# Performance work log

Hardware: AMD Instinct MI355X
Metric: run time of the kernel (lower is better)

## Reference

```python
import jax, jax.numpy as jnp
import numpy as np
import math

B, T, C = 2, 1024, 1024
H = 16
HS = C // H          # head size 64
ROT = HS // 2        # rotary dims 32
TT = 1024            # ctx_len
FFN = 4 * C
EPS = 1e-6


def _layernorm(x, g, b):
    m = jnp.mean(x, -1, keepdims=True)
    v = jnp.mean((x - m) ** 2, -1, keepdims=True)
    return (x - m) * jax.lax.rsqrt(v + EPS) * g + b


def _time_shift_half(x):
    # ZeroPad2d((0,0,1,-1)) applied to first half of channels: shift by one step in time
    c = x.shape[-1]
    a = jnp.pad(x[:, :, : c // 2], ((0, 0), (1, 0), (0, 0)))[:, :-1, :]
    return jnp.concatenate([a, x[:, :, c // 2 :]], axis=-1)


def _rotate_half(x):
    x1, x2 = jnp.split(x, 2, axis=-1)
    return jnp.concatenate([-x2, x1], axis=-1)


def _rotary_cos_sin(t_len, rot, base):
    inv_freq = 1.0 / (base ** (jnp.arange(0, rot, 2, dtype=jnp.float32) / rot))
    freqs = jnp.arange(t_len, dtype=jnp.float32)[:, None] * inv_freq[None, :]
    emb = jnp.concatenate([freqs, freqs], axis=-1)  # (T, rot)
    return jnp.cos(emb), jnp.sin(emb)


def _build_w(time_w, time_alpha, time_beta, t_len):
    # faithful translation of the pad/tile/reshape circulant trick
    w = jnp.pad(time_w, ((0, 0), (0, TT)))            # (H, 2TT)
    w = jnp.tile(w, (1, TT))                          # (H, 2TT*TT)
    w = w[:, :-TT].reshape(-1, TT, 2 * TT - 1)        # (H, TT, 2TT-1)
    w = w[:, :, TT - 1 :]                             # (H, TT, TT)
    return w[:, :t_len, :t_len] * time_alpha[:, :, :t_len] * time_beta[:, :t_len, :]


def setup_inputs() -> dict:
    key = jax.random.key(0)
    ks = jax.random.split(key, 24)
    s = 0.02
    d = {
        "x": jax.random.normal(ks[0], (B, T, C), jnp.float32),
        "ln1_g": jnp.ones((C,), jnp.float32),
        "ln1_b": jnp.zeros((C,), jnp.float32),
        "Wq": jax.random.normal(ks[1], (C, C), jnp.float32) * s,
        "bq": jnp.zeros((C,), jnp.float32),
        "Wk": jax.random.normal(ks[2], (C, C), jnp.float32) * s,
        "bk": jnp.zeros((C,), jnp.float32),
        "Wv": jax.random.normal(ks[3], (C, C), jnp.float32) * s,
        "bv": jnp.zeros((C,), jnp.float32),
        "Wo": jax.random.normal(ks[4], (C, C), jnp.float32) * s,
        "bo": jnp.zeros((C,), jnp.float32),
        "time_w": 1.0 + 0.01 * jax.random.normal(ks[5], (H, TT), jnp.float32),
        "time_alpha": 1.0 + 0.01 * jax.random.normal(ks[6], (H, 1, TT), jnp.float32),
        "time_beta": 1.0 + 0.01 * jax.random.normal(ks[7], (H, TT, 1), jnp.float32),
        "time_gamma": 1.0 + 0.01 * jax.random.normal(ks[8], (TT, 1), jnp.float32),
        "Wmix": jnp.eye(H, dtype=jnp.float32) + 0.01 * jax.random.normal(ks[9], (H, H), jnp.float32),
        "ln2_g": jnp.ones((C,), jnp.float32),
        "ln2_b": jnp.zeros((C,), jnp.float32),
        "Wgk": jax.random.normal(ks[10], (C, FFN), jnp.float32) * s,
        "bgk": jnp.zeros((FFN,), jnp.float32),
        "Wgv": jax.random.normal(ks[11], (C, FFN), jnp.float32) * s,
        "bgv": jnp.zeros((FFN,), jnp.float32),
        "Wgw": jax.random.normal(ks[12], (FFN, C), jnp.float32) * s,
        "bgw": jnp.zeros((C,), jnp.float32),
    }
    return d


def _block(x, ln1_g, ln1_b, Wq, bq, Wk, bk, Wv, bv, Wo, bo,
           time_w, time_alpha, time_beta, time_gamma, Wmix,
           ln2_g, ln2_b, Wgk, bgk, Wgv, bgv, Wgw, bgw):
    b, t, c = x.shape
    # ---- MHA_pro attention sublayer (pre-LN residual) ----
    xs = _time_shift_half(_layernorm(x, ln1_g, ln1_b))
    q = (xs @ Wq + bq).reshape(b, t, H, HS).transpose(0, 2, 1, 3)  # bhtd
    k = (xs @ Wk + bk).reshape(b, t, H, HS).transpose(0, 2, 1, 3)
    v = (xs @ Wv + bv).reshape(b, t, H, HS).transpose(0, 2, 1, 3)
    qr, qp = q[..., :ROT], q[..., ROT:]
    kr, kp = k[..., :ROT], k[..., ROT:]
    cos, sin = _rotary_cos_sin(t, ROT, float(TT))  # base = ctx_len
    qr = qr * cos + _rotate_half(qr) * sin
    kr = kr * cos + _rotate_half(kr) * sin
    q = jnp.concatenate([qr, qp], axis=-1)
    k = jnp.concatenate([kr, kp], axis=-1)
    att = jnp.einsum("bhtd,bhud->bhtu", q, k) * (1.0 / math.sqrt(HS))
    causal = jnp.tril(jnp.ones((t, t), bool))
    att = jnp.where(causal, att, -jnp.inf)
    att = jax.nn.softmax(att, axis=-1)
    w = _build_w(time_w, time_alpha, time_beta, t)  # (H, T, T)
    att = att * w[None]
    att = jnp.einsum("ij,bjtu->bitu", Wmix, att)  # 1x1 conv head mix
    y = jnp.einsum("bhtu,bhud->bhtd", att, v)
    y = y.transpose(0, 2, 1, 3).reshape(b, t, c)
    y = (y @ Wo + bo) * time_gamma[:t, :]
    x = x + y
    # ---- GeGLU MLP sublayer (pre-LN residual) ----
    xm = _layernorm(x, ln2_g, ln2_b)
    kk = xm @ Wgk + bgk
    vv = xm @ Wgv + bgv
    y2 = (jax.nn.gelu(kk, approximate=False) * vv) @ Wgw + bgw
    return x + y2


def reference(x, ln1_g, ln1_b, Wq, bq, Wk, bk, Wv, bv, Wo, bo,
              time_w, time_alpha, time_beta, time_gamma, Wmix,
              ln2_g, ln2_b, Wgk, bgk, Wgv, bgv, Wgw, bgw):
    return _block(x, ln1_g, ln1_b, Wq, bq, Wk, bk, Wv, bv, Wo, bo,
                  time_w, time_alpha, time_beta, time_gamma, Wmix,
                  ln2_g, ln2_b, Wgk, bgk, Wgv, bgv, Wgw, bgw)
```

## Files before the change

kernel.cpp:

```cpp
#include <hip/hip_runtime.h>
#include <math.h>

typedef unsigned short u16;
typedef short s16x8 __attribute__((ext_vector_type(8)));
typedef float f32x4 __attribute__((ext_vector_type(4)));

#define TB 2
#define TSEQ 1024
#define CC 1024
#define NH 16
#define HSZ 64
#define FFN 4096
#define MROWS (TB*TSEQ)

#define GLOAD16(g, l) __builtin_amdgcn_global_load_lds( \
    (const __attribute__((address_space(1))) unsigned*)(g), \
    (__attribute__((address_space(3))) unsigned*)(l), 16, 0, 0)

__device__ __forceinline__ float bf2f(u16 u){
  union { unsigned u; float f; } c; c.u = ((unsigned)u) << 16; return c.f;
}
__device__ __forceinline__ u16 f2bf(float f){
  union { float f; unsigned u; } c; c.f = f;
  unsigned u = c.u;
  u += 0x7fffu + ((u >> 16) & 1);
  return (u16)(u >> 16);
}
__device__ __forceinline__ float ldin(const void* p, size_t i, int bf){
  return bf ? bf2f(((const u16*)p)[i]) : ((const float*)p)[i];
}

__global__ void k_flag(const unsigned* __restrict__ g, int* __restrict__ flag){
  if (threadIdx.x == 0) *flag = (g[0] == 0x3F800000u) ? 0 : 1;
}

__global__ void k_transpose_cvt(const void* __restrict__ in, u16* __restrict__ out,
                                int R, int Cc, const int* __restrict__ flagp){
  int bf = *flagp;
  __shared__ u16 tile[32][33];
  int bx = blockIdx.x * 32, by = blockIdx.y * 32;
  int tx = threadIdx.x & 31, ty = threadIdx.x >> 5;
  #pragma unroll
  for (int i = 0; i < 32; i += 8)
    tile[ty + i][tx] = f2bf(ldin(in, (size_t)(by + ty + i) * Cc + bx + tx, bf));
  __syncthreads();
  #pragma unroll
  for (int i = 0; i < 32; i += 8)
    out[(size_t)(bx + ty + i) * R + by + tx] = tile[tx][ty + i];
}

__global__ void k_cvt(const void* __restrict__ in, u16* __restrict__ out, int n,
                      const int* __restrict__ flagp){
  int bf = *flagp;
  int i = blockIdx.x * 256 + threadIdx.x;
  if (i < n) out[i] = f2bf(ldin(in, i, bf));
}

__global__ void k_tw8(const void* __restrict__ tw, u16* __restrict__ tw8,
                      const int* __restrict__ flagp){
  int bf = *flagp;
  int idx = blockIdx.x*256 + threadIdx.x;
  int s = idx >> 14;
  int h = (idx >> 10) & 15;
  int k = idx & 1023;
  float v = (k + s < 1024) ? ldin(tw, h*1024 + k + s, bf) : 0.f;
  tw8[idx] = f2bf(v);
}

__global__ void k_ln1_shift(const void* __restrict__ x, const void* __restrict__ g,
                            const void* __restrict__ bta, u16* __restrict__ xs,
                            const int* __restrict__ flagp){
  int bf = *flagp;
  int row = blockIdx.x;
  int t = row & (TSEQ - 1);
  int tid = threadIdx.x;
  float v[4]; float s = 0.f, ss = 0.f;
  #pragma unroll
  for (int i = 0; i < 4; i++){
    v[i] = ldin(x, (size_t)row * CC + tid*4 + i, bf);
    s += v[i]; ss += v[i]*v[i];
  }
  __shared__ float rs[256], rss[256];
  rs[tid] = s; rss[tid] = ss; __syncthreads();
  for (int o = 128; o > 0; o >>= 1){ if (tid < o){ rs[tid] += rs[tid+o]; rss[tid] += rss[tid+o]; } __syncthreads(); }
  float mean = rs[0] * (1.0f/CC);
  float var  = rss[0] * (1.0f/CC) - mean*mean;
  float inv  = rsqrtf(var + 1e-6f);
  #pragma unroll
  for (int i = 0; i < 4; i++){
    int c = tid*4 + i;
    float o = (v[i]-mean)*inv*ldin(g, c, bf) + ldin(bta, c, bf);
    u16 ob = f2bf(o);
    if (c >= CC/2)            xs[(size_t)row*CC + c] = ob;
    else if (t < TSEQ-1)      xs[(size_t)(row+1)*CC + c] = ob;
  }
  if (t == 0 && tid < 128){
    #pragma unroll
    for (int i = 0; i < 4; i++) xs[(size_t)row*CC + tid*4 + i] = 0;
  }
}

__global__ void k_ln2(const float* __restrict__ x1, const void* __restrict__ g,
                      const void* __restrict__ bta, u16* __restrict__ xm,
                      const int* __restrict__ flagp){
  int bf = *flagp;
  int row = blockIdx.x;
  int tid = threadIdx.x;
  const float* xr = x1 + (size_t)row * CC;
  float v[4]; float s = 0.f, ss = 0.f;
  #pragma unroll
  for (int i = 0; i < 4; i++){ v[i] = xr[tid*4 + i]; s += v[i]; ss += v[i]*v[i]; }
  __shared__ float rs[256], rss[256];
  rs[tid] = s; rss[tid] = ss; __syncthreads();
  for (int o = 128; o > 0; o >>= 1){ if (tid < o){ rs[tid] += rs[tid+o]; rss[tid] += rss[tid+o]; } __syncthreads(); }
  float mean = rs[0] * (1.0f/CC);
  float var  = rss[0] * (1.0f/CC) - mean*mean;
  float inv  = rsqrtf(var + 1e-6f);
  #pragma unroll
  for (int i = 0; i < 4; i++){
    int c = tid*4 + i;
    xm[(size_t)row*CC + c] = f2bf((v[i]-mean)*inv*ldin(g, c, bf) + ldin(bta, c, bf));
  }
}

__global__ void k_rotary(u16* __restrict__ qkv){
  int idx = blockIdx.x*256 + threadIdx.x;
  int i = idx & 15;
  int h = (idx >> 4) & (NH-1);
  int row = idx >> 8;
  int t = row & (TSEQ-1);
  float invf = exp2f(-0.625f * (float)i);
  float ang = (float)t * invf;
  float cs = cosf(ang), sn = sinf(ang);
  size_t base = (size_t)row * (3*CC);
  u16* qp = qkv + base + h*HSZ;
  float a = bf2f(qp[i]), b2 = bf2f(qp[i+16]);
  qp[i]    = f2bf(a*cs - b2*sn);
  qp[i+16] = f2bf(b2*cs + a*sn);
  u16* kp = qkv + base + CC + h*HSZ;
  a = bf2f(kp[i]); b2 = bf2f(kp[i+16]);
  kp[i]    = f2bf(a*cs - b2*sn);
  kp[i+16] = f2bf(b2*cs + a*sn);
}

__global__ __launch_bounds__(256) void k_qk(
    const u16* __restrict__ qkv, u16* __restrict__ att)
{
  int m0 = blockIdx.y * 128;
  int n0 = blockIdx.x * 128;
  if (n0 > m0) return;
  int bh = blockIdx.z; int b = bh >> 4, h = bh & 15;
  __shared__ u16 As[128*32];
  __shared__ u16 Bs[128*32];
  int tid = threadIdx.x;
  int w = tid >> 6;
  int lane = tid & 63;
  int wm = (w >> 1) * 64, wn = (w & 1) * 64;
  f32x4 acc[4][4];
  #pragma unroll
  for (int i = 0; i < 4; i++)
    #pragma unroll
    for (int j = 0; j < 4; j++) acc[i][j] = (f32x4){0.f,0.f,0.f,0.f};

  int rr = lane >> 2;
  int cc = lane & 3;
  const u16* gA0 = qkv + (size_t)(b*TSEQ + m0 + w*32 + rr)*(3*CC) + h*HSZ + cc*8;
  const u16* gA1 = gA0 + (size_t)16*(3*CC);
  const u16* gB0 = qkv + (size_t)(b*TSEQ + n0 + w*32 + rr)*(3*CC) + CC + h*HSZ + cc*8;
  const u16* gB1 = gB0 + (size_t)16*(3*CC);
  u16* lA0 = As + (w*32)*32;
  u16* lA1 = As + (w*32+16)*32;
  u16* lB0 = Bs + (w*32)*32;
  u16* lB1 = Bs + (w*32+16)*32;
  int quad = lane >> 4;
  int l15 = lane & 15;

  #pragma unroll
  for (int k0 = 0; k0 < HSZ; k0 += 32){
    __syncthreads();
    GLOAD16(gA0 + k0, lA0);
    GLOAD16(gA1 + k0, lA1);
    GLOAD16(gB0 + k0, lB0);
    GLOAD16(gB1 + k0, lB1);
    __syncthreads();
    s16x8 af[4], bfr[4];
    #pragma unroll
    for (int i = 0; i < 4; i++){
      af[i]  = *(s16x8*)&As[(wm + i*16 + l15)*32 + quad*8];
      bfr[i] = *(s16x8*)&Bs[(wn + i*16 + l15)*32 + quad*8];
    }
    #pragma unroll
    for (int mi = 0; mi < 4; mi++)
      #pragma unroll
      for (int ni = 0; ni < 4; ni++)
        acc[mi][ni] = __builtin_amdgcn_mfma_f32_16x16x32_bf16(af[mi], bfr[ni], acc[mi][ni], 0, 0, 0);
  }

  #pragma unroll
  for (int mi = 0; mi < 4; mi++){
    int rowb = m0 + wm + mi*16 + quad*4;
    #pragma unroll
    for (int ni = 0; ni < 4; ni++){
      int col = n0 + wn + ni*16 + l15;
      #pragma unroll
      for (int r = 0; r < 4; r++){
        int t = rowb + r;
        att[((size_t)bh*TSEQ + t)*TSEQ + col] = f2bf(acc[mi][ni][r] * 0.125f);
      }
    }
  }
}

__global__ __launch_bounds__(256) void k_softmix(
    u16* __restrict__ att, const u16* __restrict__ tw8, const u16* __restrict__ al16,
    const u16* __restrict__ be16, const void* __restrict__ wmix,
    const int* __restrict__ flagp)
{
  int bf = *flagp;
  int bt = blockIdx.x;
  int t = bt & (TSEQ-1);
  int b = bt >> 10;
  int tid = threadIdx.x;
  int wv = tid >> 6;
  int lane = tid & 63;
  int tile_end = ((t >> 7) + 1) << 7;
  int nchunk = (t >> 9) + 1;
  int sh = (TSEQ-1 - t) & 7;
  int base = (TSEQ-1 - t) - sh;
  __shared__ __align__(16) u16 P[NH][TSEQ];
  __shared__ float wm[NH*NH];
  if (tid < NH*NH) wm[tid] = ldin(wmix, tid, bf);

  #pragma unroll
  for (int hi = 0; hi < 4; hi++){
    int h = wv*4 + hi;
    const u16* srow = att + ((size_t)(b*NH + h)*TSEQ + t)*TSEQ;
    const u16* twp  = tw8 + ((size_t)sh*NH + h)*TSEQ + base;
    const u16* alp  = al16 + h*TSEQ;
    float v[16];
    float lmax = -1e30f;
    for (int r = 0; r < nchunk; r++){
      int ub = lane*8 + r*512;
      uint4 pk = *(const uint4*)(srow + ub);
      const u16* pe = (const u16*)&pk;
      #pragma unroll
      for (int e = 0; e < 8; e++){
        float s = bf2f(pe[e]);
        if (ub + e > t) s = -1e30f;
        v[r*8+e] = s;
        lmax = fmaxf(lmax, s);
      }
    }
    #pragma unroll
    for (int o = 32; o > 0; o >>= 1) lmax = fmaxf(lmax, __shfl_xor(lmax, o));
    float lsum = 0.f;
    for (int r = 0; r < nchunk; r++){
      #pragma unroll
      for (int e = 0; e < 8; e++){
        float p = __expf(v[r*8+e] - lmax);
        v[r*8+e] = p; lsum += p;
      }
    }
    #pragma unroll
    for (int o = 32; o > 0; o >>= 1) lsum += __shfl_xor(lsum, o);
    float btv = bf2f(be16[h*TSEQ + t]);
    float inv = btv / lsum;
    for (int r = 0; r < nchunk; r++){
      int ub = lane*8 + r*512;
      uint4 wk = *(const uint4*)(twp + ub);
      uint4 ak = *(const uint4*)(alp + ub);
      const u16* we = (const u16*)&wk;
      const u16* ae = (const u16*)&ak;
      u16 tmp[8];
      #pragma unroll
      for (int e = 0; e < 8; e++){
        float p = v[r*8+e] * inv * bf2f(we[e]) * bf2f(ae[e]);
        tmp[e] = f2bf(p);
      }
      *(uint4*)&P[h][ub] = *(uint4*)tmp;
    }
  }
  __syncthreads();

  int u0 = tid * 4;
  if (u0 < tile_end){
    #pragma unroll
    for (int half = 0; half < 2; half++){
      float acc[8][4];
      #pragma unroll
      for (int i = 0; i < 8; i++)
        #pragma unroll
        for (int k = 0; k < 4; k++) acc[i][k] = 0.f;
      #pragma unroll
      for (int j = 0; j < 16; j++){
        uint2 pk = *(const uint2*)&P[j][u0];
        float p0 = bf2f((u16)(pk.x & 0xffff)), p1 = bf2f((u16)(pk.x >> 16));
        float p2 = bf2f((u16)(pk.y & 0xffff)), p3 = bf2f((u16)(pk.y >> 16));
        #pragma unroll
        for (int i2 = 0; i2 < 8; i2++){
          float w = wm[(half*8 + i2)*NH + j];
          acc[i2][0] += w*p0; acc[i2][1] += w*p1; acc[i2][2] += w*p2; acc[i2][3] += w*p3;
        }
      }
      #pragma unroll
      for (int i2 = 0; i2 < 8; i2++){
        int i = half*8 + i2;
        u16 tmp[4] = {f2bf(acc[i2][0]), f2bf(acc[i2][1]), f2bf(acc[i2][2]), f2bf(acc[i2][3])};
        *(uint2*)(att + ((size_t)(b*NH + i)*TSEQ + t)*TSEQ + u0) = *(uint2*)tmp;
      }
    }
  }
}

__global__ void k_vt(const u16* __restrict__ qkv, u16* __restrict__ vt){
  __shared__ u16 tile[32][33];
  int bh = blockIdx.z; int b = bh >> 4, h = bh & 15;
  int u0 = blockIdx.x * 32, d0 = blockIdx.y * 32;
  int tx = threadIdx.x & 31, ty = threadIdx.x >> 5;
  #pragma unroll
  for (int i = 0; i < 32; i += 8)
    tile[ty + i][tx] = qkv[(size_t)(b*TSEQ + u0 + ty + i)*(3*CC) + 2*CC + h*HSZ + d0 + tx];
  __syncthreads();
  #pragma unroll
  for (int i = 0; i < 32; i += 8)
    vt[((size_t)bh*HSZ + d0 + ty + i)*TSEQ + u0 + tx] = tile[tx][ty + i];
}

__global__ void k_gelumul(const u16* __restrict__ kkvv, u16* __restrict__ hh){
  int idx = blockIdx.x*256 + threadIdx.x;
  int m = idx >> 9;
  int j = (idx & 511) * 8;
  uint4 kk4 = *(const uint4*)(kkvv + (size_t)m*(2*FFN) + j);
  uint4 vv4 = *(const uint4*)(kkvv + (size_t)m*(2*FFN) + FFN + j);
  const u16* ks = (const u16*)&kk4;
  const u16* vs = (const u16*)&vv4;
  u16 out[8];
  #pragma unroll
  for (int e = 0; e < 8; e++){
    float kk = bf2f(ks[e]), vv = bf2f(vs[e]);
    float ge = 0.5f*kk*(1.0f + erff(kk*0.70710678f));
    out[e] = f2bf(ge*vv);
  }
  *(uint4*)(hh + (size_t)m*FFN + j) = *(uint4*)out;
}

__global__ __launch_bounds__(256) void k_gemm(
    const u16* __restrict__ A, const u16* __restrict__ Bt,
    const u16* __restrict__ bias, int M, int N, int K, int mode,
    void* __restrict__ outp, const void* __restrict__ xres,
    const float* __restrict__ resf, const u16* __restrict__ gamma,
    float* __restrict__ partial, const int* __restrict__ flagp)
{
  int bf = *flagp;
  __shared__ u16 As[128*32];
  __shared__ u16 Bs[128*32];
  int tid = threadIdx.x;
  int m0 = blockIdx.y * 128;
  int n0 = blockIdx.x * 128;
  int nz = gridDim.z;
  int kper = K / nz;
  int kbeg = blockIdx.z * kper;
  int kend = kbeg + kper;
  int w = tid >> 6;
  int lane = tid & 63;
  int wm = (w >> 1) * 64, wn = (w & 1) * 64;
  f32x4 acc[4][4];
  #pragma unroll
  for (int i = 0; i < 4; i++)
    #pragma unroll
    for (int j = 0; j < 4; j++) acc[i][j] = (f32x4){0.f,0.f,0.f,0.f};

  int rr = lane >> 2;
  int cc = lane & 3;
  const u16* gA0 = A  + (size_t)(m0 + w*32 + rr)*K + cc*8;
  const u16* gA1 = gA0 + (size_t)16*K;
  const u16* gB0 = Bt + (size_t)(n0 + w*32 + rr)*K + cc*8;
  const u16* gB1 = gB0 + (size_t)16*K;
  u16* lA0 = As + (w*32)*32;
  u16* lA1 = As + (w*32+16)*32;
  u16* lB0 = Bs + (w*32)*32;
  u16* lB1 = Bs + (w*32+16)*32;
  int quad = lane >> 4;
  int l15 = lane & 15;

  for (int k0 = kbeg; k0 < kend; k0 += 32){
    __syncthreads();
    GLOAD16(gA0 + k0, lA0);
    GLOAD16(gA1 + k0, lA1);
    GLOAD16(gB0 + k0, lB0);
    GLOAD16(gB1 + k0, lB1);
    __syncthreads();
    s16x8 af[4], bfr[4];
    #pragma unroll
    for (int i = 0; i < 4; i++){
      af[i]  = *(s16x8*)&As[(wm + i*16 + l15)*32 + quad*8];
      bfr[i] = *(s16x8*)&Bs[(wn + i*16 + l15)*32 + quad*8];
    }
    #pragma unroll
    for (int mi = 0; mi < 4; mi++)
      #pragma unroll
      for (int ni = 0; ni < 4; ni++)
        acc[mi][ni] = __builtin_amdgcn_mfma_f32_16x16x32_bf16(af[mi], bfr[ni], acc[mi][ni], 0, 0, 0);
  }

  if (nz > 1){
    float* pout = partial + (size_t)blockIdx.z * M * N;
    #pragma unroll
    for (int mi = 0; mi < 4; mi++){
      int rowb = m0 + wm + mi*16 + quad*4;
      #pragma unroll
      for (int ni = 0; ni < 4; ni++){
        int col = n0 + wn + ni*16 + l15;
        #pragma unroll
        for (int r = 0; r < 4; r++)
          pout[(size_t)(rowb + r) * N + col] = acc[mi][ni][r];
      }
    }
    return;
  }

  #pragma unroll
  for (int mi = 0; mi < 4; mi++){
    int rowb = m0 + wm + mi*16 + quad*4;
    #pragma unroll
    for (int ni = 0; ni < 4; ni++){
      int col = n0 + wn + ni*16 + l15;
      float bv = bf2f(bias[col]);
      #pragma unroll
      for (int r = 0; r < 4; r++){
        int row = rowb + r;
        float val = acc[mi][ni][r] + bv;
        size_t idx = (size_t)row * N + col;
        if (mode == 0){
          ((u16*)outp)[idx] = f2bf(val);
        } else if (mode == 1){
          int t = row & (TSEQ-1);
          ((float*)outp)[idx] = ldin(xres, idx, bf) + val * bf2f(gamma[t]);
        } else {
          float o = resf[idx] + val;
          if (bf) ((u16*)outp)[idx] = f2bf(o);
          else    ((float*)outp)[idx] = o;
        }
      }
    }
  }
}

__global__ void k_reduceK(const float* __restrict__ partial, int nsplit,
                          int M, int N, const u16* __restrict__ bias, int mode,
                          void* __restrict__ outp, const void* __restrict__ xres,
                          const float* __restrict__ resf, const u16* __restrict__ gamma,
                          const int* __restrict__ flagp){
  int bf = *flagp;
  int idx = blockIdx.x*256 + threadIdx.x;
  int row = idx / (N/4);
  int c0  = (idx % (N/4)) * 4;
  size_t base = (size_t)row * N + c0;
  float v[4] = {0.f, 0.f, 0.f, 0.f};
  for (int s = 0; s < nsplit; s++){
    const float4 p = *(const float4*)(partial + (size_t)s * M * N + base);
    v[0] += p.x; v[1] += p.y; v[2] += p.z; v[3] += p.w;
  }
  #pragma unroll
  for (int e = 0; e < 4; e++) v[e] += bf2f(bias[c0 + e]);
  if (mode == 1){
    int t = row & (TSEQ-1);
    float gm = bf2f(gamma[t]);
    float o[4];
    #pragma unroll
    for (int e = 0; e < 4; e++) o[e] = ldin(xres, base + e, bf) + v[e] * gm;
    *(float4*)((float*)outp + base) = (float4){o[0], o[1], o[2], o[3]};
  } else {
    float o[4];
    #pragma unroll
    for (int e = 0; e < 4; e++) o[e] = resf[base + e] + v[e];
    if (bf){
      u16 tmp[4] = {f2bf(o[0]), f2bf(o[1]), f2bf(o[2]), f2bf(o[3])};
      *(uint2*)((u16*)outp + base) = *(uint2*)tmp;
    } else {
      *(float4*)((float*)outp + base) = (float4){o[0], o[1], o[2], o[3]};
    }
  }
}

__global__ __launch_bounds__(256) void k_pv(
    const u16* __restrict__ att, const u16* __restrict__ vt, u16* __restrict__ y)
{
  __shared__ u16 As[128*32];
  __shared__ u16 Bs[64*32];
  int tid = threadIdx.x;
  int bh = blockIdx.y; int b = bh >> 4, h = bh & 15;
  int m0 = blockIdx.x * 128;
  const u16* A  = att + (size_t)bh * TSEQ * TSEQ;
  const u16* Bt = vt  + (size_t)bh * HSZ * TSEQ;
  int w = tid >> 6;
  int lane = tid & 63;
  int wm = (w >> 1) * 64, wn = (w & 1) * 32;
  f32x4 acc[4][2];
  #pragma unroll
  for (int i = 0; i < 4; i++){ acc[i][0] = (f32x4){0,0,0,0}; acc[i][1] = (f32x4){0,0,0,0}; }

  int rr = lane >> 2;
  int cc = lane & 3;
  const u16* gA0 = A + (size_t)(m0 + w*32 + rr)*TSEQ + cc*8;
  const u16* gA1 = gA0 + (size_t)16*TSEQ;
  const u16* gB0 = Bt + (size_t)(w*16 + rr)*TSEQ + cc*8;
  u16* lA0 = As + (w*32)*32;
  u16* lA1 = As + (w*32+16)*32;
  u16* lB0 = Bs + (w*16)*32;
  int quad = lane >> 4;
  int l15 = lane & 15;
  int kend = m0 + 128;

  for (int k0 = 0; k0 < kend; k0 += 32){
    __syncthreads();
    GLOAD16(gA0 + k0, lA0);
    GLOAD16(gA1 + k0, lA1);
    GLOAD16(gB0 + k0, lB0);
    __syncthreads();
    s16x8 af[4], bfr[2];
    #pragma unroll
    for (int i = 0; i < 4; i++)
      af[i] = *(s16x8*)&As[(wm + i*16 + l15)*32 + quad*8];
    #pragma unroll
    for (int i = 0; i < 2; i++)
      bfr[i] = *(s16x8*)&Bs[(wn + i*16 + l15)*32 + quad*8];
    #pragma unroll
    for (int mi = 0; mi < 4; mi++)
      #pragma unroll
      for (int ni = 0; ni < 2; ni++)
        acc[mi][ni] = __builtin_amdgcn_mfma_f32_16x16x32_bf16(af[mi], bfr[ni], acc[mi][ni], 0, 0, 0);
  }

  #pragma unroll
  for (int mi = 0; mi < 4; mi++){
    int rowb = m0 + wm + mi*16 + quad*4;
    #pragma unroll
    for (int ni = 0; ni < 2; ni++){
      int col = wn + ni*16 + l15;
      #pragma unroll
      for (int r = 0; r < 4; r++){
        int t = rowb + r;
        y[(size_t)(b*TSEQ + t)*CC + h*HSZ + col] = f2bf(acc[mi][ni][r]);
      }
    }
  }
}

extern "C" void kernel_launch(void* const* d_in, const int* in_sizes, int n_in,
                              void* d_out, int out_size, void* d_ws, size_t ws_size,
                              hipStream_t stream){
  const void* x     = d_in[0];
  const void* ln1g  = d_in[1];
  const void* ln1b  = d_in[2];
  const void* Wq    = d_in[3];
  const void* bq    = d_in[4];
  const void* Wk    = d_in[5];
  const void* bk    = d_in[6];
  const void* Wv    = d_in[7];
  const void* bv    = d_in[8];
  const void* Wo    = d_in[9];
  const void* bo    = d_in[10];
  const void* timew = d_in[11];
  const void* alpha = d_in[12];
  const void* beta  = d_in[13];
  const void* gamma = d_in[14];
  const void* Wmix  = d_in[15];
  const void* ln2g  = d_in[16];
  const void* ln2b  = d_in[17];
  const void* Wgk   = d_in[18];
  const void* bgk   = d_in[19];
  const void* Wgv   = d_in[20];
  const void* bgv   = d_in[21];
  const void* Wgw   = d_in[22];
  const void* bgw   = d_in[23];

  char* ws = (char*)d_ws;
  size_t off = 0;
  auto carve = [&](size_t bytes)->char*{
    char* p = ws + off; off = (off + bytes + 255) & ~(size_t)255; return p;
  };
  int*  FLAG   = (int*)carve(256);
  u16*  WT_QKV = (u16*)carve(3072ull*1024*2);
  u16*  WT_O   = (u16*)carve(1024ull*1024*2);
  u16*  WT_G   = (u16*)carve(8192ull*1024*2);
  u16*  WT_W   = (u16*)carve(1024ull*4096*2);
  u16*  B_QKV  = (u16*)carve(3072*2);
  u16*  B_G    = (u16*)carve(8192*2);
  u16*  B_O    = (u16*)carve(1024*2);
  u16*  B_W    = (u16*)carve(1024*2);
  u16*  GMA    = (u16*)carve(1024*2);
  u16*  TW8    = (u16*)carve(8ull*16*1024*2 + 4096);
  u16*  AL16   = (u16*)carve(16*1024*2);
  u16*  BE16   = (u16*)carve(16*1024*2);
  u16*  XS     = (u16*)carve((size_t)MROWS*CC*2);
  u16*  QKV    = (u16*)carve((size_t)MROWS*3*CC*2);
  u16*  ATT    = (u16*)carve((size_t)TB*NH*TSEQ*TSEQ*2);
  u16*  VT     = (u16*)carve((size_t)TB*NH*HSZ*TSEQ*2);
  u16*  Y      = (u16*)carve((size_t)MROWS*CC*2);
  float* X1    = (float*)carve((size_t)MROWS*CC*4);
  u16*  XM     = (u16*)carve((size_t)MROWS*CC*2);
  u16*  KKVV   = (u16*)carve((size_t)MROWS*2*FFN*2);
  u16*  HH     = (u16*)carve((size_t)MROWS*FFN*2);
  float* PART  = (float*)ATT;
  (void)ws_size; (void)in_sizes; (void)n_in; (void)out_size;

  k_flag<<<1,64,0,stream>>>((const unsigned*)ln1g, FLAG);

  k_transpose_cvt<<<dim3(32,32),256,0,stream>>>(Wq, WT_QKV,                1024, 1024, FLAG);
  k_transpose_cvt<<<dim3(32,32),256,0,stream>>>(Wk, WT_QKV + 1024*1024,    1024, 1024, FLAG);
  k_transpose_cvt<<<dim3(32,32),256,0,stream>>>(Wv, WT_QKV + 2*1024*1024,  1024, 1024, FLAG);
  k_transpose_cvt<<<dim3(32,32),256,0,stream>>>(Wo, WT_O,                  1024, 1024, FLAG);
  k_transpose_cvt<<<dim3(128,32),256,0,stream>>>(Wgk, WT_G,                1024, 4096, FLAG);
  k_transpose_cvt<<<dim3(128,32),256,0,stream>>>(Wgv, WT_G + 4096ull*1024, 1024, 4096, FLAG);
  k_transpose_cvt<<<dim3(32,128),256,0,stream>>>(Wgw, WT_W,                4096, 1024, FLAG);
  k_cvt<<<4,256,0,stream>>>(bq, B_QKV,        1024, FLAG);
  k_cvt<<<4,256,0,stream>>>(bk, B_QKV + 1024, 1024, FLAG);
  k_cvt<<<4,256,0,stream>>>(bv, B_QKV + 2048, 1024, FLAG);
  k_cvt<<<16,256,0,stream>>>(bgk, B_G,        4096, FLAG);
  k_cvt<<<16,256,0,stream>>>(bgv, B_G + 4096, 4096, FLAG);
  k_cvt<<<4,256,0,stream>>>(bo,  B_O, 1024, FLAG);
  k_cvt<<<4,256,0,stream>>>(bgw, B_W, 1024, FLAG);
  k_cvt<<<4,256,0,stream>>>(gamma, GMA, 1024, FLAG);
  k_tw8<<<512,256,0,stream>>>(timew, TW8, FLAG);
  k_cvt<<<64,256,0,stream>>>(alpha, AL16, 16384, FLAG);
  k_cvt<<<64,256,0,stream>>>(beta,  BE16, 16384, FLAG);

  k_ln1_shift<<<MROWS,256,0,stream>>>(x, ln1g, ln1b, XS, FLAG);
  k_gemm<<<dim3(24,16),256,0,stream>>>(XS, WT_QKV, B_QKV, MROWS, 3072, 1024, 0,
                                       QKV, nullptr, nullptr, nullptr, nullptr, FLAG);
  k_rotary<<<2048,256,0,stream>>>(QKV);
  k_qk<<<dim3(8,8,TB*NH),256,0,stream>>>(QKV, ATT);
  k_softmix<<<TB*TSEQ,256,0,stream>>>(ATT, TW8, AL16, BE16, Wmix, FLAG);
  k_vt<<<dim3(32,2,32),256,0,stream>>>(QKV, VT);
  k_pv<<<dim3(8,32),256,0,stream>>>(ATT, VT, Y);

  k_gemm<<<dim3(8,16,2),256,0,stream>>>(Y, WT_O, B_O, MROWS, 1024, 1024, 1,
                                        nullptr, nullptr, nullptr, nullptr, PART, FLAG);
  k_reduceK<<<MROWS*1024/(4*256),256,0,stream>>>(PART, 2, MROWS, 1024, B_O, 1,
                                                 X1, x, nullptr, GMA, FLAG);

  k_ln2<<<MROWS,256,0,stream>>>(X1, ln2g, ln2b, XM, FLAG);
  k_gemm<<<dim3(64,16),256,0,stream>>>(XM, WT_G, B_G, MROWS, 8192, 1024, 0,
                                       KKVV, nullptr, nullptr, nullptr, nullptr, FLAG);
  k_gelumul<<<(MROWS*FFN)/(256*8),256,0,stream>>>(KKVV, HH);

  k_gemm<<<dim3(8,16,4),256,0,stream>>>(HH, WT_W, B_W, MROWS, 1024, 4096, 2,
                                        nullptr, nullptr, nullptr, nullptr, PART, FLAG);
  k_reduceK<<<MROWS*1024/(4*256),256,0,stream>>>(PART, 4, MROWS, 1024, B_W, 2,
                                                 d_out, nullptr, X1, nullptr, FLAG);
}
```

Baseline: 477.6 us.

## Fuse GeGLU into gate GEMM epilogue and LN2 into split-K reduction

Interleaves the Wgk and Wgv weight columns in 64-wide blocks so each 128-column GEMM tile holds matching k and v halves. The GELU-times-v product is then computed in the GEMM epilogue through shared memory, which removes the KKVV intermediate buffer and the separate gelumul kernel. The split-K reduction for the output projection also applies the residual, gamma and LayerNorm 2, replacing two kernels with one. The cost is an extra 34KB of LDS in the gate GEMM, which may lower occupancy.

```diff
diff --git a/kernel.cpp b/kernel.cpp
--- a/kernel.cpp
+++ b/kernel.cpp
@@ -35,7 +35,8 @@
 }
 
 __global__ void k_transpose_cvt(const void* __restrict__ in, u16* __restrict__ out,
-                                int R, int Cc, const int* __restrict__ flagp){
+                                int R, int Cc, const int* __restrict__ flagp,
+                                int nremap, int half){
   int bf = *flagp;
   __shared__ u16 tile[32][33];
   int bx = blockIdx.x * 32, by = blockIdx.y * 32;
@@ -45,8 +46,11 @@
     tile[ty + i][tx] = f2bf(ldin(in, (size_t)(by + ty + i) * Cc + bx + tx, bf));
   __syncthreads();
   #pragma unroll
-  for (int i = 0; i < 32; i += 8)
-    out[(size_t)(bx + ty + i) * R + by + tx] = tile[tx][ty + i];
+  for (int i = 0; i < 32; i += 8){
+    int n = bx + ty + i;
+    int np = nremap ? (((n >> 6) << 7) + half*64 + (n & 63)) : n;
+    out[(size_t)np * R + by + tx] = tile[tx][ty + i];
+  }
 }
 
 __global__ void k_cvt(const void* __restrict__ in, u16* __restrict__ out, int n,
@@ -54,6 +58,16 @@
   int bf = *flagp;
   int i = blockIdx.x * 256 + threadIdx.x;
   if (i < n) out[i] = f2bf(ldin(in, i, bf));
+}
+
+__global__ void k_cvt_g2(const void* __restrict__ bgk, const void* __restrict__ bgv,
+                         u16* __restrict__ out, const int* __restrict__ flagp){
+  int bf = *flagp;
+  int idx = blockIdx.x*256 + threadIdx.x;
+  int j = idx & 4095;
+  int isv = idx >> 12;
+  float v = isv ? ldin(bgv, j, bf) : ldin(bgk, j, bf);
+  out[(j >> 6)*128 + isv*64 + (j & 63)] = f2bf(v);
 }
 
 __global__ void k_tw8(const void* __restrict__ tw, u16* __restrict__ tw8,
@@ -97,29 +111,6 @@
   if (t == 0 && tid < 128){
     #pragma unroll
     for (int i = 0; i < 4; i++) xs[(size_t)row*CC + tid*4 + i] = 0;
-  }
-}
-
-__global__ void k_ln2(const float* __restrict__ x1, const void* __restrict__ g,
-                      const void* __restrict__ bta, u16* __restrict__ xm,
-                      const int* __restrict__ flagp){
-  int bf = *flagp;
-  int row = blockIdx.x;
-  int tid = threadIdx.x;
-  const float* xr = x1 + (size_t)row * CC;
-  float v[4]; float s = 0.f, ss = 0.f;
-  #pragma unroll
-  for (int i = 0; i < 4; i++){ v[i] = xr[tid*4 + i]; s += v[i]; ss += v[i]*v[i]; }
-  __shared__ float rs[256], rss[256];
-  rs[tid] = s; rss[tid] = ss; __syncthreads();
-  for (int o = 128; o > 0; o >>= 1){ if (tid < o){ rs[tid] += rs[tid+o]; rss[tid] += rss[tid+o]; } __syncthreads(); }
-  float mean = rs[0] * (1.0f/CC);
-  float var  = rss[0] * (1.0f/CC) - mean*mean;
-  float inv  = rsqrtf(var + 1e-6f);
-  #pragma unroll
-  for (int i = 0; i < 4; i++){
-    int c = tid*4 + i;
-    xm[(size_t)row*CC + c] = f2bf((v[i]-mean)*inv*ldin(g, c, bf) + ldin(bta, c, bf));
   }
 }
 
@@ -326,29 +317,10 @@
     vt[((size_t)bh*HSZ + d0 + ty + i)*TSEQ + u0 + tx] = tile[tx][ty + i];
 }
 
-__global__ void k_gelumul(const u16* __restrict__ kkvv, u16* __restrict__ hh){
-  int idx = blockIdx.x*256 + threadIdx.x;
-  int m = idx >> 9;
-  int j = (idx & 511) * 8;
-  uint4 kk4 = *(const uint4*)(kkvv + (size_t)m*(2*FFN) + j);
-  uint4 vv4 = *(const uint4*)(kkvv + (size_t)m*(2*FFN) + FFN + j);
-  const u16* ks = (const u16*)&kk4;
-  const u16* vs = (const u16*)&vv4;
-  u16 out[8];
-  #pragma unroll
-  for (int e = 0; e < 8; e++){
-    float kk = bf2f(ks[e]), vv = bf2f(vs[e]);
-    float ge = 0.5f*kk*(1.0f + erff(kk*0.70710678f));
-    out[e] = f2bf(ge*vv);
-  }
-  *(uint4*)(hh + (size_t)m*FFN + j) = *(uint4*)out;
-}
-
 __global__ __launch_bounds__(256) void k_gemm(
     const u16* __restrict__ A, const u16* __restrict__ Bt,
     const u16* __restrict__ bias, int M, int N, int K, int mode,
-    void* __restrict__ outp, const void* __restrict__ xres,
-    const float* __restrict__ resf, const u16* __restrict__ gamma,
+    void* __restrict__ outp, const float* __restrict__ resf,
     float* __restrict__ partial, const int* __restrict__ flagp)
 {
   int bf = *flagp;
@@ -428,14 +400,11 @@
       float bv = bf2f(bias[col]);
       #pragma unroll
       for (int r = 0; r < 4; r++){
-        int row = rowb + r;
+        int rw = rowb + r;
         float val = acc[mi][ni][r] + bv;
-        size_t idx = (size_t)row * N + col;
+        size_t idx = (size_t)rw * N + col;
         if (mode == 0){
           ((u16*)outp)[idx] = f2bf(val);
-        } else if (mode == 1){
-          int t = row & (TSEQ-1);
-          ((float*)outp)[idx] = ldin(xres, idx, bf) + val * bf2f(gamma[t]);
         } else {
           float o = resf[idx] + val;
           if (bf) ((u16*)outp)[idx] = f2bf(o);
@@ -446,10 +415,136 @@
   }
 }
 
+__global__ __launch_bounds__(256) void k_gemm_gelu(
+    const u16* __restrict__ A, const u16* __restrict__ Bt,
+    const u16* __restrict__ bias, int M, int K,
+    u16* __restrict__ hh, const int* __restrict__ flagp)
+{
+  (void)flagp;
+  __shared__ u16 As[128*32];
+  __shared__ u16 Bs[128*32];
+  __shared__ float VV[128*68];
+  int tid = threadIdx.x;
+  int m0 = blockIdx.y * 128;
+  int n0 = blockIdx.x * 128;
+  int t  = blockIdx.x;
+  int w = tid >> 6;
+  int lane = tid & 63;
+  int wm = (w >> 1) * 64, wn = (w & 1) * 64;
+  f32x4 acc[4][4];
+  #pragma unroll
+  for (int i = 0; i < 4; i++)
+    #pragma unroll
+    for (int j = 0; j < 4; j++) acc[i][j] = (f32x4){0.f,0.f,0.f,0.f};
+
+  int rr = lane >> 2;
+  int cc = lane & 3;
+  const u16* gA0 = A  + (size_t)(m0 + w*32 + rr)*K + cc*8;
+  const u16* gA1 = gA0 + (size_t)16*K;
+  const u16* gB0 = Bt + (size_t)(n0 + w*32 + rr)*K + cc*8;
+  const u16* gB1 = gB0 + (size_t)16*K;
+  u16* lA0 = As + (w*32)*32;
+  u16* lA1 = As + (w*32+16)*32;
+  u16* lB0 = Bs + (w*32)*32;
+  u16* lB1 = Bs + (w*32+16)*32;
+  int quad = lane >> 4;
+  int l15 = lane & 15;
+
+  for (int k0 = 0; k0 < K; k0 += 32){
+    __syncthreads();
+    GLOAD16(gA0 + k0, lA0);
+    GLOAD16(gA1 + k0, lA1);
+    GLOAD16(gB0 + k0, lB0);
+    GLOAD16(gB1 + k0, lB1);
+    __syncthreads();
+    s16x8 af[4], bfr[4];
+    #pragma unroll
+    for (int i = 0; i < 4; i++){
+      af[i]  = *(s16x8*)&As[(wm + i*16 + l15)*32 + quad*8];
+      bfr[i] = *(s16x8*)&Bs[(wn + i*16 + l15)*32 + quad*8];
+    }
+    #pragma unroll
+    for (int mi = 0; mi < 4; mi++)
+      #pragma unroll
+      for (int ni = 0; ni < 4; ni++)
+        acc[mi][ni] = __builtin_amdgcn_mfma_f32_16x16x32_bf16(af[mi], bfr[ni], acc[mi][ni], 0, 0, 0);
+  }
+
+  if (wn == 64){
+    #pragma unroll
+    for (int mi = 0; mi < 4; mi++){
+      int rowb = wm + mi*16 + quad*4;
+      #pragma unroll
+      for (int ni = 0; ni < 4; ni++){
+        int jj = ni*16 + l15;
+        float bv = bf2f(bias[n0 + 64 + jj]);
+        #pragma unroll
+        for (int r = 0; r < 4; r++)
+          VV[(rowb + r)*68 + jj] = acc[mi][ni][r] + bv;
+      }
+    }
+  }
+  __syncthreads();
+  if (wn == 0){
+    #pragma unroll
+    for (int mi = 0; mi < 4; mi++){
+      int rowb = wm + mi*16 + quad*4;
+      #pragma unroll
+      for (int ni = 0; ni < 4; ni++){
+        int jj = ni*16 + l15;
+        float bv = bf2f(bias[n0 + jj]);
+        #pragma unroll
+        for (int r = 0; r < 4; r++){
+          int row = rowb + r;
+          float kk = acc[mi][ni][r] + bv;
+          float vv = VV[row*68 + jj];
+          float ge = 0.5f*kk*(1.0f + erff(kk*0.70710678f));
+          hh[(size_t)(m0 + row)*FFN + t*64 + jj] = f2bf(ge*vv);
+        }
+      }
+    }
+  }
+}
+
+__global__ void k_reduceLN(const float* __restrict__ partial, int nsplit, int MN1,
+                           const u16* __restrict__ bias, const void* __restrict__ xres,
+                           const u16* __restrict__ gamma, const void* __restrict__ g2,
+                           const void* __restrict__ b2, float* __restrict__ x1,
+                           u16* __restrict__ xm, const int* __restrict__ flagp){
+  int bf = *flagp;
+  int row = blockIdx.x;
+  int tid = threadIdx.x;
+  int c0 = tid*4;
+  size_t base = (size_t)row * CC + c0;
+  float v[4] = {0.f,0.f,0.f,0.f};
+  for (int s = 0; s < nsplit; s++){
+    const float4 p = *(const float4*)(partial + (size_t)s * MN1 + base);
+    v[0] += p.x; v[1] += p.y; v[2] += p.z; v[3] += p.w;
+  }
+  float gm = bf2f(gamma[row & (TSEQ-1)]);
+  float s = 0.f, ss = 0.f;
+  #pragma unroll
+  for (int e = 0; e < 4; e++){
+    v[e] = ldin(xres, base + e, bf) + (v[e] + bf2f(bias[c0 + e])) * gm;
+    s += v[e]; ss += v[e]*v[e];
+  }
+  *(float4*)(x1 + base) = (float4){v[0], v[1], v[2], v[3]};
+  __shared__ float rs[256], rss[256];
+  rs[tid] = s; rss[tid] = ss; __syncthreads();
+  for (int o = 128; o > 0; o >>= 1){ if (tid < o){ rs[tid] += rs[tid+o]; rss[tid] += rss[tid+o]; } __syncthreads(); }
+  float mean = rs[0] * (1.0f/CC);
+  float var  = rss[0] * (1.0f/CC) - mean*mean;
+  float inv  = rsqrtf(var + 1e-6f);
+  u16 tmp[4];
+  #pragma unroll
+  for (int e = 0; e < 4; e++)
+    tmp[e] = f2bf((v[e]-mean)*inv*ldin(g2, c0+e, bf) + ldin(b2, c0+e, bf));
+  *(uint2*)(xm + base) = *(uint2*)tmp;
+}
+
 __global__ void k_reduceK(const float* __restrict__ partial, int nsplit,
-                          int M, int N, const u16* __restrict__ bias, int mode,
-                          void* __restrict__ outp, const void* __restrict__ xres,
-                          const float* __restrict__ resf, const u16* __restrict__ gamma,
+                          int M, int N, const u16* __restrict__ bias,
+                          void* __restrict__ outp, const float* __restrict__ resf,
                           const int* __restrict__ flagp){
   int bf = *flagp;
   int idx = blockIdx.x*256 + threadIdx.x;
@@ -461,25 +556,14 @@
     const float4 p = *(const float4*)(partial + (size_t)s * M * N + base);
     v[0] += p.x; v[1] += p.y; v[2] += p.z; v[3] += p.w;
   }
-  #pragma unroll
-  for (int e = 0; e < 4; e++) v[e] += bf2f(bias[c0 + e]);
-  if (mode == 1){
-    int t = row & (TSEQ-1);
-    float gm = bf2f(gamma[t]);
-    float o[4];
-    #pragma unroll
-    for (int e = 0; e < 4; e++) o[e] = ldin(xres, base + e, bf) + v[e] * gm;
+  float o[4];
+  #pragma unroll
+  for (int e = 0; e < 4; e++) o[e] = resf[base + e] + v[e] + bf2f(bias[c0 + e]);
+  if (bf){
+    u16 tmp[4] = {f2bf(o[0]), f2bf(o[1]), f2bf(o[2]), f2bf(o[3])};
+    *(uint2*)((u16*)outp + base) = *(uint2*)tmp;
+  } else {
     *(float4*)((float*)outp + base) = (float4){o[0], o[1], o[2], o[3]};
-  } else {
-    float o[4];
-    #pragma unroll
-    for (int e = 0; e < 4; e++) o[e] = resf[base + e] + v[e];
-    if (bf){
-      u16 tmp[4] = {f2bf(o[0]), f2bf(o[1]), f2bf(o[2]), f2bf(o[3])};
-      *(uint2*)((u16*)outp + base) = *(uint2*)tmp;
-    } else {
-      *(float4*)((float*)outp + base) = (float4){o[0], o[1], o[2], o[3]};
-    }
   }
 }
 
@@ -583,10 +667,10 @@
   int*  FLAG   = (int*)carve(256);
   u16*  WT_QKV = (u16*)carve(3072ull*1024*2);
   u16*  WT_O   = (u16*)carve(1024ull*1024*2);
-  u16*  WT_G   = (u16*)carve(8192ull*1024*2);
+  u16*  WT_G2  = (u16*)carve(8192ull*1024*2);
   u16*  WT_W   = (u16*)carve(1024ull*4096*2);
   u16*  B_QKV  = (u16*)carve(3072*2);
-  u16*  B_G    = (u16*)carve(8192*2);
+  u16*  B_G2   = (u16*)carve(8192*2);
   u16*  B_O    = (u16*)carve(1024*2);
   u16*  B_W    = (u16*)carve(1024*2);
   u16*  GMA    = (u16*)carve(1024*2);
@@ -600,25 +684,23 @@
   u16*  Y      = (u16*)carve((size_t)MROWS*CC*2);
   float* X1    = (float*)carve((size_t)MROWS*CC*4);
   u16*  XM     = (u16*)carve((size_t)MROWS*CC*2);
-  u16*  KKVV   = (u16*)carve((size_t)MROWS*2*FFN*2);
   u16*  HH     = (u16*)carve((size_t)MROWS*FFN*2);
   float* PART  = (float*)ATT;
   (void)ws_size; (void)in_sizes; (void)n_in; (void)out_size;
 
   k_flag<<<1,64,0,stream>>>((const unsigned*)ln1g, FLAG);
 
-  k_transpose_cvt<<<dim3(32,32),256,0,stream>>>(Wq, WT_QKV,                1024, 1024, FLAG);
-  k_transpose_cvt<<<dim3(32,32),256,0,stream>>>(Wk, WT_QKV + 1024*1024,    1024, 1024, FLAG);
-  k_transpose_cvt<<<dim3(32,32),256,0,stream>>>(Wv, WT_QKV + 2*1024*1024,  1024, 1024, FLAG);
-  k_transpose_cvt<<<dim3(32,32),256,0,stream>>>(Wo, WT_O,                  1024, 1024, FLAG);
-  k_transpose_cvt<<<dim3(128,32),256,0,stream>>>(Wgk, WT_G,                1024, 4096, FLAG);
-  k_transpose_cvt<<<dim3(128,32),256,0,stream>>>(Wgv, WT_G + 4096ull*1024, 1024, 4096, FLAG);
-  k_transpose_cvt<<<dim3(32,128),256,0,stream>>>(Wgw, WT_W,                4096, 1024, FLAG);
+  k_transpose_cvt<<<dim3(32,32),256,0,stream>>>(Wq, WT_QKV,               1024, 1024, FLAG, 0, 0);
+  k_transpose_cvt<<<dim3(32,32),256,0,stream>>>(Wk, WT_QKV + 1024*1024,   1024, 1024, FLAG, 0, 0);
+  k_transpose_cvt<<<dim3(32,32),256,0,stream>>>(Wv, WT_QKV + 2*1024*1024, 1024, 1024, FLAG, 0, 0);
+  k_transpose_cvt<<<dim3(32,32),256,0,stream>>>(Wo, WT_O,                 1024, 1024, FLAG, 0, 0);
+  k_transpose_cvt<<<dim3(128,32),256,0,stream>>>(Wgk, WT_G2,              1024, 4096, FLAG, 1, 0);
+  k_transpose_cvt<<<dim3(128,32),256,0,stream>>>(Wgv, WT_G2,              1024, 4096, FLAG, 1, 1);
+  k_transpose_cvt<<<dim3(32,128),256,0,stream>>>(Wgw, WT_W,               4096, 1024, FLAG, 0, 0);
   k_cvt<<<4,256,0,stream>>>(bq, B_QKV,        1024, FLAG);
   k_cvt<<<4,256,0,stream>>>(bk, B_QKV + 1024, 1024, FLAG);
   k_cvt<<<4,256,0,stream>>>(bv, B_QKV + 2048, 1024, FLAG);
-  k_cvt<<<16,256,0,stream>>>(bgk, B_G,        4096, FLAG);
-  k_cvt<<<16,256,0,stream>>>(bgv, B_G + 4096, 4096, FLAG);
+  k_cvt_g2<<<32,256,0,stream>>>(bgk, bgv, B_G2, FLAG);
   k_cvt<<<4,256,0,stream>>>(bo,  B_O, 1024, FLAG);
   k_cvt<<<4,256,0,stream>>>(bgw, B_W, 1024, FLAG);
   k_cvt<<<4,256,0,stream>>>(gamma, GMA, 1024, FLAG);
@@ -628,25 +710,22 @@
 
   k_ln1_shift<<<MROWS,256,0,stream>>>(x, ln1g, ln1b, XS, FLAG);
   k_gemm<<<dim3(24,16),256,0,stream>>>(XS, WT_QKV, B_QKV, MROWS, 3072, 1024, 0,
-                                       QKV, nullptr, nullptr, nullptr, nullptr, FLAG);
+                                       QKV, nullptr, nullptr, FLAG);
   k_rotary<<<2048,256,0,stream>>>(QKV);
   k_qk<<<dim3(8,8,TB*NH),256,0,stream>>>(QKV, ATT);
   k_softmix<<<TB*TSEQ,256,0,stream>>>(ATT, TW8, AL16, BE16, Wmix, FLAG);
   k_vt<<<dim3(32,2,32),256,0,stream>>>(QKV, VT);
   k_pv<<<dim3(8,32),256,0,stream>>>(ATT, VT, Y);
 
-  k_gemm<<<dim3(8,16,2),256,0,stream>>>(Y, WT_O, B_O, MROWS, 1024, 1024, 1,
-                                        nullptr, nullptr, nullptr, nullptr, PART, FLAG);
-  k_reduceK<<<MROWS*1024/(4*256),256,0,stream>>>(PART, 2, MROWS, 1024, B_O, 1,
-                                                 X1, x, nullptr, GMA, FLAG);
-
-  k_ln2<<<MROWS,256,0,stream>>>(X1, ln2g, ln2b, XM, FLAG);
-  k_gemm<<<dim3(64,16),256,0,stream>>>(XM, WT_G, B_G, MROWS, 8192, 1024, 0,
-                                       KKVV, nullptr, nullptr, nullptr, nullptr, FLAG);
-  k_gelumul<<<(MROWS*FFN)/(256*8),256,0,stream>>>(KKVV, HH);
+  k_gemm<<<dim3(8,16,2),256,0,stream>>>(Y, WT_O, B_O, MROWS, 1024, 1024, 0,
+                                        nullptr, nullptr, PART, FLAG);
+  k_reduceLN<<<MROWS,256,0,stream>>>(PART, 2, MROWS*1024, B_O, x, GMA,
+                                     ln2g, ln2b, X1, XM, FLAG);
+
+  k_gemm_gelu<<<dim3(64,16),256,0,stream>>>(XM, WT_G2, B_G2, MROWS, 1024, HH, FLAG);
 
   k_gemm<<<dim3(8,16,4),256,0,stream>>>(HH, WT_W, B_W, MROWS, 1024, 4096, 2,
-                                        nullptr, nullptr, nullptr, nullptr, PART, FLAG);
-  k_reduceK<<<MROWS*1024/(4*256),256,0,stream>>>(PART, 4, MROWS, 1024, B_W, 2,
-                                                 d_out, nullptr, X1, nullptr, FLAG);
-}
+                                        nullptr, nullptr, PART, FLAG);
+  k_reduceK<<<MROWS*1024/(4*256),256,0,stream>>>(PART, 4, MROWS, 1024, B_W,
+                                                 d_out, X1, FLAG);
+}
```

Result: slower. 512.0 us (+7.2%).
